# Kernel tuning notes

Measured on AMD Instinct MI355X. Metric: run time of the kernel, lower is better.

The kernel has to match this reference:

```python
import jax, jax.numpy as jnp
import numpy as np

NUM_NODES = 100000
NUM_EDGES = 3200000
NUM_GRAPHS = 512
IN_DIM, OUT_DIM = 128, 16
DIMS = [IN_DIM, 32, 48, 64]


def glorot(key, shape):
    lim = float(np.sqrt(6.0 / (shape[0] + shape[1])))
    return jax.random.uniform(key, shape, jnp.float32, -lim, lim)


def setup_inputs() -> dict:
    key = jax.random.key(0)
    ks = jax.random.split(key, 12)
    x = jax.random.normal(ks[0], (NUM_NODES, IN_DIM), jnp.float32)
    edge_index = jax.random.randint(ks[1], (2, NUM_EDGES), 0, NUM_NODES, jnp.int64)
    batch = jnp.sort(jax.random.randint(ks[2], (NUM_NODES,), 0, NUM_GRAPHS, jnp.int64))
    params = {}
    for i in range(3):
        params[f"W{i+1}"] = glorot(ks[3 + i], (DIMS[i], DIMS[i + 1]))
        params[f"b{i+1}"] = jnp.zeros((DIMS[i + 1],), jnp.float32)
    params["fc1_w"] = glorot(ks[6], (64, 32))
    params["fc1_b"] = jnp.zeros((32,), jnp.float32)
    params["fc2_w"] = glorot(ks[7], (32, OUT_DIM))
    params["fc2_b"] = jnp.zeros((OUT_DIM,), jnp.float32)
    return {"x": x, "edge_index": edge_index, "batch": batch, **params}


def gcn_conv(x, W, b, src, dst, deg_inv_sqrt):
    # h = x @ W; aggregate with symmetric normalization + self loops (PyG GCNConv)
    h = x @ W  # [N, out]
    norm = deg_inv_sqrt[src] * deg_inv_sqrt[dst]  # [E]
    msg = h[src] * norm[:, None]  # [E, out]  (gather)
    agg = jnp.zeros_like(h).at[dst].add(msg)  # scatter-add to targets
    self_loop = h * (deg_inv_sqrt * deg_inv_sqrt)[:, None]
    return agg + self_loop + b


def reference(x, edge_index, batch, W1, b1, W2, b2, W3, b3, fc1_w, fc1_b, fc2_w, fc2_b):
    src, dst = edge_index[0], edge_index[1]
    n = x.shape[0]
    # degree with self loops: deg[i] = in-degree + 1
    deg = jnp.zeros((n,), jnp.float32).at[dst].add(1.0) + 1.0
    dis = jax.lax.rsqrt(deg)
    h = jax.nn.relu(gcn_conv(x, W1, b1, src, dst, dis))
    h = jax.nn.relu(gcn_conv(h, W2, b2, src, dst, dis))
    h = jax.nn.relu(gcn_conv(h, W3, b3, src, dst, dis))
    # global mean pool per graph
    sums = jax.ops.segment_sum(h, batch, num_segments=NUM_GRAPHS)
    cnts = jax.ops.segment_sum(jnp.ones((n,), jnp.float32), batch, num_segments=NUM_GRAPHS)
    pooled = sums / jnp.maximum(cnts, 1.0)[:, None]  # [G, 64]
    z = jax.nn.relu(pooled @ fc1_w + fc1_b)
    logits = z @ fc2_w + fc2_b
    return jax.nn.softmax(logits, axis=1)
```

## Files before the change

### kernel.cpp

```cpp
#include <hip/hip_runtime.h>
#include <hip/hip_fp16.h>

static constexpr int NN = 100000;
static constexpr int NE = 3200000;
static constexpr int NG = 512;
static constexpr int NCB = 196;
static constexpr int CHK = 8192;
static constexpr int NCH = (NE + CHK - 1) / CHK;
static constexpr int NCNT = NCB * NCH;
static constexpr int SCAN_BLK = 2048;
static constexpr int NSB = (NCNT + SCAN_BLK - 1) / SCAN_BLK;

typedef float f32x2 __attribute__((ext_vector_type(2)));

__device__ __forceinline__ void acc_fp8x4(unsigned v, float* a) {
    f32x2 lo = __builtin_amdgcn_cvt_pk_f32_fp8((int)v, false);
    f32x2 hi = __builtin_amdgcn_cvt_pk_f32_fp8((int)v, true);
    a[0] += lo.x; a[1] += lo.y; a[2] += hi.x; a[3] += hi.y;
}
__device__ __forceinline__ void set_fp8x4(unsigned v, float* a) {
    f32x2 lo = __builtin_amdgcn_cvt_pk_f32_fp8((int)v, false);
    f32x2 hi = __builtin_amdgcn_cvt_pk_f32_fp8((int)v, true);
    a[0] = lo.x; a[1] = lo.y; a[2] = hi.x; a[3] = hi.y;
}
__device__ __forceinline__ unsigned pack_fp8x4(float a, float b, float c, float d) {
    int p = __builtin_amdgcn_cvt_pk_fp8_f32(a, b, 0, false);
    p = __builtin_amdgcn_cvt_pk_fp8_f32(c, d, p, true);
    return (unsigned)p;
}

__global__ __launch_bounds__(256) void k_histC(const int* __restrict__ dst,
                                               int* __restrict__ cntC, int e) {
    __shared__ int h[NCB];
    for (int i = threadIdx.x; i < NCB; i += 256) h[i] = 0;
    __syncthreads();
    const int s = blockIdx.x * CHK, eend = min(s + CHK, e);
    for (int i = s + threadIdx.x; i < eend; i += 256)
        atomicAdd(&h[dst[i] >> 9], 1);
    __syncthreads();
    for (int i = threadIdx.x; i < NCB; i += 256)
        cntC[(size_t)i * NCH + blockIdx.x] = h[i];
}

__global__ __launch_bounds__(256) void k_scanA(const int* __restrict__ in,
                                               int* __restrict__ out,
                                               int* __restrict__ bsum, int n) {
    __shared__ int s[256];
    const int tid = threadIdx.x;
    const int base = blockIdx.x * SCAN_BLK + tid * 8;
    int v[8], t = 0;
#pragma unroll
    for (int c = 0; c < 8; c++) {
        int idx = base + c;
        v[c] = (idx < n) ? in[idx] : 0;
        t += v[c];
    }
    s[tid] = t;
    __syncthreads();
    for (int off = 1; off < 256; off <<= 1) {
        int x = (tid >= off) ? s[tid - off] : 0;
        __syncthreads();
        s[tid] += x;
        __syncthreads();
    }
    if (tid == 255) bsum[blockIdx.x] = s[255];
    int run = s[tid] - t;
#pragma unroll
    for (int c = 0; c < 8; c++) {
        int idx = base + c;
        if (idx < n) out[idx] = run;
        run += v[c];
    }
}

__global__ __launch_bounds__(256) void k_scanB(int* __restrict__ bsum, int nb) {
    __shared__ int s[256];
    const int tid = threadIdx.x;
    int v = (tid < nb) ? bsum[tid] : 0;
    s[tid] = v;
    __syncthreads();
    for (int off = 1; off < 256; off <<= 1) {
        int x = (tid >= off) ? s[tid - off] : 0;
        __syncthreads();
        s[tid] += x;
        __syncthreads();
    }
    if (tid < nb) bsum[tid] = s[tid] - v;
}

__global__ __launch_bounds__(256) void k_scanC(int* __restrict__ out,
                                               const int* __restrict__ bsum, int n) {
    int i = blockIdx.x * 256 + threadIdx.x;
    if (i < n) out[i] += bsum[i / SCAN_BLK];
}

__global__ __launch_bounds__(256) void k_scatC(const int* __restrict__ src,
                                               const int* __restrict__ dst,
                                               const int* __restrict__ scC,
                                               unsigned* __restrict__ tmp, int e) {
    __shared__ int cur[NCB];
    for (int i = threadIdx.x; i < NCB; i += 256)
        cur[i] = scC[(size_t)i * NCH + blockIdx.x];
    __syncthreads();
    const int s = blockIdx.x * CHK, eend = min(s + CHK, e);
    for (int i = s + threadIdx.x; i < eend; i += 256) {
        int d = dst[i];
        int p = atomicAdd(&cur[d >> 9], 1);
        tmp[p] = ((unsigned)(d & 511) << 17) | (unsigned)src[i];
    }
}

__global__ __launch_bounds__(1024) void k_fill512(const unsigned* __restrict__ tmp,
                                                  const int* __restrict__ scC,
                                                  int* __restrict__ csr,
                                                  int* __restrict__ degi,
                                                  int* __restrict__ offs,
                                                  float* __restrict__ dis,
                                                  int n, int etotal) {
    __shared__ int cnt[512];
    __shared__ int s[512];
    __shared__ int cur[512];
    const int b = blockIdx.x, tid = threadIdx.x;
    if (tid < 512) cnt[tid] = 0;
    const int e0 = scC[(size_t)b * NCH];
    const int e1 = (b + 1 < NCB) ? scC[(size_t)(b + 1) * NCH] : etotal;
    __syncthreads();
    for (int e = e0 + tid; e < e1; e += 1024)
        atomicAdd(&cnt[tmp[e] >> 17], 1);
    __syncthreads();
    int v = 0;
    if (tid < 512) { v = cnt[tid]; s[tid] = v; }
    __syncthreads();
    for (int off = 1; off < 512; off <<= 1) {
        int x = 0;
        if (tid < 512 && tid >= off) x = s[tid - off];
        __syncthreads();
        if (tid < 512) s[tid] += x;
        __syncthreads();
    }
    if (tid < 512) {
        int c = e0 + s[tid] - v;
        cur[tid] = c;
        int node = b * 512 + tid;
        if (node < n) {
            degi[node] = v;
            offs[node] = c;
            dis[node] = rsqrtf((float)v + 1.0f);
        }
    }
    __syncthreads();
    for (int e = e0 + tid; e < e1; e += 1024) {
        unsigned pk = tmp[e];
        int p = atomicAdd(&cur[pk >> 17], 1);
        csr[p] = (int)(pk & 0x1FFFFu);
    }
}

__global__ __launch_bounds__(256) void k_gemm1(const float* __restrict__ X,
                                               const float* __restrict__ W,
                                               const float* __restrict__ dis,
                                               unsigned* __restrict__ H, int n) {
    constexpr int IN = 128, ROWS = 32;
    __shared__ float sW[IN * 32];
    __shared__ float sX[ROWS][IN];
    const int tid = threadIdx.x;
    for (int i = tid; i < IN * 32; i += 256) sW[i] = W[i];
    const int row0 = blockIdx.x * ROWS;
    for (int i = tid; i < ROWS * IN; i += 256) {
        int r = row0 + i / IN;
        sX[i / IN][i % IN] = (r < n) ? X[(size_t)r * IN + i % IN] : 0.f;
    }
    __syncthreads();
    const int lr = tid >> 3;
    const int cg = tid & 7;
    const int gr = row0 + lr;
    float acc[4] = {0.f, 0.f, 0.f, 0.f};
#pragma unroll 8
    for (int k = 0; k < IN; k++) {
        float xv = sX[lr][k];
#pragma unroll
        for (int c = 0; c < 4; c++)
            acc[c] = fmaf(xv, sW[k * 32 + 4 * cg + c], acc[c]);
    }
    if (gr < n) {
        float dd = dis[gr];
        H[(size_t)gr * 8 + cg] =
            pack_fp8x4(acc[0] * dd, acc[1] * dd, acc[2] * dd, acc[3] * dd);
    }
}

__global__ __launch_bounds__(256) void k_pull2(
        const unsigned* __restrict__ Hp, const int* __restrict__ offs,
        const int* __restrict__ degi, const int* __restrict__ csr,
        const float* __restrict__ dis, const float* __restrict__ b,
        unsigned* __restrict__ A, int n) {
    const int group = threadIdx.x >> 3, j0 = threadIdx.x & 7;
    const int d = blockIdx.x * 32 + group;
    if (d >= n) return;
    float acc[4];
    set_fp8x4(Hp[(size_t)d * 8 + j0], acc);
    int e = offs[d];
    const int end = e + degi[d];
    for (; e + 3 < end; e += 4) {
        unsigned v0 = Hp[(size_t)csr[e] * 8 + j0];
        unsigned v1 = Hp[(size_t)csr[e + 1] * 8 + j0];
        unsigned v2 = Hp[(size_t)csr[e + 2] * 8 + j0];
        unsigned v3 = Hp[(size_t)csr[e + 3] * 8 + j0];
        acc_fp8x4(v0, acc); acc_fp8x4(v1, acc);
        acc_fp8x4(v2, acc); acc_fp8x4(v3, acc);
    }
    for (; e < end; e++) acc_fp8x4(Hp[(size_t)csr[e] * 8 + j0], acc);
    const float dd = dis[d];
    float r[4];
#pragma unroll
    for (int c = 0; c < 4; c++)
        r[c] = fmaxf(fmaf(acc[c], dd, b[4 * j0 + c]), 0.f) * dd;
    A[(size_t)d * 8 + j0] = pack_fp8x4(r[0], r[1], r[2], r[3]);
}

__global__ __launch_bounds__(256) void k_pullmm32(
        const unsigned* __restrict__ Hp, const int* __restrict__ offs,
        const int* __restrict__ degi, const int* __restrict__ csr,
        const float* __restrict__ dis, const float* __restrict__ W,
        const float* __restrict__ b, unsigned* __restrict__ A, int n) {
    __shared__ float sW[32 * 48];
    __shared__ float rows[32][32];
    __shared__ float aout[32][48];
    for (int i = threadIdx.x; i < 32 * 48; i += 256) sW[i] = W[i];
    const int group = threadIdx.x >> 3, j0 = threadIdx.x & 7;
    const int d = blockIdx.x * 32 + group;
    if (d < n) {
        float acc[4];
        set_fp8x4(Hp[(size_t)d * 8 + j0], acc);
        int e = offs[d];
        const int end = e + degi[d];
        for (; e + 3 < end; e += 4) {
            unsigned v0 = Hp[(size_t)csr[e] * 8 + j0];
            unsigned v1 = Hp[(size_t)csr[e + 1] * 8 + j0];
            unsigned v2 = Hp[(size_t)csr[e + 2] * 8 + j0];
            unsigned v3 = Hp[(size_t)csr[e + 3] * 8 + j0];
            acc_fp8x4(v0, acc); acc_fp8x4(v1, acc);
            acc_fp8x4(v2, acc); acc_fp8x4(v3, acc);
        }
        for (; e < end; e++) acc_fp8x4(Hp[(size_t)csr[e] * 8 + j0], acc);
        const float dd = dis[d];
#pragma unroll
        for (int c = 0; c < 4; c++) rows[group][4 * j0 + c] = acc[c] * dd;
    }
    __syncthreads();
    const int row0 = blockIdx.x * 32;
#pragma unroll
    for (int o = 0; o < 6; o++) {
        int idx = o * 256 + threadIdx.x;
        int nl = idx / 48, col = idx % 48;
        float s = b[col];
#pragma unroll
        for (int k = 0; k < 32; k++)
            s = fmaf(rows[nl][k], sW[k * 48 + col], s);
        aout[nl][col] = fmaxf(s, 0.f) * dis[min(row0 + nl, n - 1)];
    }
    __syncthreads();
    for (int idx = threadIdx.x; idx < 32 * 16; idx += 256) {
        int nl = idx >> 4, cg = idx & 15;
        int gr = row0 + nl;
        if (gr < n) {
            unsigned p = 0;
            if (cg < 12)
                p = pack_fp8x4(aout[nl][4 * cg], aout[nl][4 * cg + 1],
                               aout[nl][4 * cg + 2], aout[nl][4 * cg + 3]);
            A[(size_t)gr * 16 + cg] = p;
        }
    }
}

__global__ __launch_bounds__(256) void k_pullmm48(
        const uint2* __restrict__ Hp, const int* __restrict__ offs,
        const int* __restrict__ degi, const int* __restrict__ csr,
        const float* __restrict__ dis, const float* __restrict__ W,
        const float* __restrict__ b, __half* __restrict__ A, int n) {
    __shared__ float sW[48 * 64];
    __shared__ float rows[32][48];
    for (int i = threadIdx.x; i < 48 * 64; i += 256) sW[i] = W[i];
    const int group = threadIdx.x >> 3, j0 = threadIdx.x & 7;
    const int d = blockIdx.x * 32 + group;
    if (d < n) {
        float acc[8];
        uint2 sv = Hp[(size_t)d * 8 + j0];
        set_fp8x4(sv.x, acc); set_fp8x4(sv.y, acc + 4);
        int e = offs[d];
        const int end = e + degi[d];
        for (; e + 3 < end; e += 4) {
            uint2 v0 = Hp[(size_t)csr[e] * 8 + j0];
            uint2 v1 = Hp[(size_t)csr[e + 1] * 8 + j0];
            uint2 v2 = Hp[(size_t)csr[e + 2] * 8 + j0];
            uint2 v3 = Hp[(size_t)csr[e + 3] * 8 + j0];
            acc_fp8x4(v0.x, acc); acc_fp8x4(v0.y, acc + 4);
            acc_fp8x4(v1.x, acc); acc_fp8x4(v1.y, acc + 4);
            acc_fp8x4(v2.x, acc); acc_fp8x4(v2.y, acc + 4);
            acc_fp8x4(v3.x, acc); acc_fp8x4(v3.y, acc + 4);
        }
        for (; e < end; e++) {
            uint2 v = Hp[(size_t)csr[e] * 8 + j0];
            acc_fp8x4(v.x, acc); acc_fp8x4(v.y, acc + 4);
        }
        const float dd = dis[d];
        if (j0 < 6) {
#pragma unroll
            for (int c = 0; c < 8; c++) rows[group][8 * j0 + c] = acc[c] * dd;
        }
    }
    __syncthreads();
    const int row0 = blockIdx.x * 32;
#pragma unroll
    for (int o = 0; o < 8; o++) {
        int idx = o * 256 + threadIdx.x;
        int nl = idx >> 6, col = idx & 63;
        int gr = row0 + nl;
        if (gr < n) {
            float s = b[col];
#pragma unroll
            for (int k = 0; k < 48; k++)
                s = fmaf(rows[nl][k], sW[k * 64 + col], s);
            A[(size_t)gr * 64 + col] = __float2half(s);
        }
    }
}

__global__ __launch_bounds__(256) void k_bounds(const int* __restrict__ batch,
                                                int* __restrict__ bounds,
                                                int n, int ngr) {
    int g = blockIdx.x * 256 + threadIdx.x;
    if (g > ngr) return;
    if (g == ngr) { bounds[g] = n; return; }
    int lo = 0, hi = n;
    while (lo < hi) {
        int mid = (lo + hi) >> 1;
        if (batch[mid] < g) lo = mid + 1; else hi = mid;
    }
    bounds[g] = lo;
}

__global__ __launch_bounds__(256) void k_pool(const __half* __restrict__ A3,
                                              const int* __restrict__ bounds,
                                              float* __restrict__ pooled) {
    const int g = blockIdx.x;
    const int j = threadIdx.x & 63, rl = threadIdx.x >> 6;
    const int s = bounds[g], e = bounds[g + 1];
    float sum = 0.f;
    for (int node = s + rl; node < e; node += 4)
        sum += fmaxf(__half2float(A3[(size_t)node * 64 + j]), 0.f);
    __shared__ float red[4][64];
    red[rl][j] = sum;
    __syncthreads();
    if (rl == 0)
        pooled[g * 64 + j] = (red[0][j] + red[1][j] + red[2][j] + red[3][j]) /
                             fmaxf((float)(e - s), 1.f);
}

__global__ __launch_bounds__(64) void k_head(
        const float* __restrict__ pooled,
        const float* __restrict__ f1w, const float* __restrict__ f1b,
        const float* __restrict__ f2w, const float* __restrict__ f2b,
        float* __restrict__ out) {
    int g = blockIdx.x;
    int t = threadIdx.x;
    __shared__ float p[64], z[32], lg[16];
    p[t] = pooled[g * 64 + t];
    __syncthreads();
    if (t < 32) {
        float acc = f1b[t];
        for (int j = 0; j < 64; j++) acc = fmaf(p[j], f1w[j * 32 + t], acc);
        z[t] = fmaxf(acc, 0.f);
    }
    __syncthreads();
    if (t < 16) {
        float acc = f2b[t];
        for (int k = 0; k < 32; k++) acc = fmaf(z[k], f2w[k * 16 + t], acc);
        lg[t] = acc;
    }
    __syncthreads();
    if (t < 16) {
        float m = lg[0];
        for (int i = 1; i < 16; i++) m = fmaxf(m, lg[i]);
        float s = 0.f;
        for (int i = 0; i < 16; i++) s += expf(lg[i] - m);
        out[g * 16 + t] = expf(lg[t] - m) / s;
    }
}

extern "C" void kernel_launch(void* const* d_in, const int* in_sizes, int n_in,
                              void* d_out, int out_size, void* d_ws, size_t ws_size,
                              hipStream_t stream) {
    (void)in_sizes; (void)n_in; (void)out_size; (void)ws_size;
    const float* x     = (const float*)d_in[0];
    const int*   ei    = (const int*)d_in[1];
    const int*   batch = (const int*)d_in[2];
    const float* W1 = (const float*)d_in[3];
    const float* b1 = (const float*)d_in[4];
    const float* W2 = (const float*)d_in[5];  const float* b2 = (const float*)d_in[6];
    const float* W3 = (const float*)d_in[7];  const float* b3 = (const float*)d_in[8];
    const float* f1w = (const float*)d_in[9]; const float* f1b = (const float*)d_in[10];
    const float* f2w = (const float*)d_in[11];const float* f2b = (const float*)d_in[12];
    float* out = (float*)d_out;

    const int* src = ei;
    const int* dst = ei + NE;

    float* ws = (float*)d_ws;
    size_t o = 0;
    float* dis    = ws + o; o += NN;
    int*   degi   = (int*)(ws + o); o += NN;
    int*   offs   = (int*)(ws + o); o += NN;
    int*   cntC   = (int*)(ws + o); o += 76640;
    int*   scC    = (int*)(ws + o); o += 76640;
    int*   bsum   = (int*)(ws + o); o += 48;
    int*   bounds = (int*)(ws + o); o += 528;
    float* pooled = ws + o; o += (size_t)NG * 64;
    int*   csr    = (int*)(ws + o); o += NE;
    unsigned* TA  = (unsigned*)(ws + o); o += NE;
    unsigned* H1  = (unsigned*)(ws + o); o += NN * 8;
    unsigned* H2  = (unsigned*)(ws + o); o += NN * 8;
    unsigned* H3  = (unsigned*)(ws + o); o += NN * 16;

    unsigned* tmp = TA;
    __half*   A3  = (__half*)TA;

    k_histC<<<NCH, 256, 0, stream>>>(dst, cntC, NE);
    k_scanA<<<NSB, 256, 0, stream>>>(cntC, scC, bsum, NCNT);
    k_scanB<<<1, 256, 0, stream>>>(bsum, NSB);
    k_scanC<<<(NCNT + 255) / 256, 256, 0, stream>>>(scC, bsum, NCNT);
    k_scatC<<<NCH, 256, 0, stream>>>(src, dst, scC, tmp, NE);
    k_fill512<<<NCB, 1024, 0, stream>>>(tmp, scC, csr, degi, offs, dis, NN, NE);

    const int PGRID = (NN + 31) / 32;

    k_gemm1<<<(NN + 31) / 32, 256, 0, stream>>>(x, W1, dis, H1, NN);
    k_pull2<<<PGRID, 256, 0, stream>>>(H1, offs, degi, csr, dis, b1, H2, NN);

    k_pullmm32<<<PGRID, 256, 0, stream>>>(H2, offs, degi, csr, dis, W2, b2, H3, NN);

    k_pullmm48<<<PGRID, 256, 0, stream>>>(
        (const uint2*)H3, offs, degi, csr, dis, W3, b3, A3, NN);

    k_bounds<<<(NG + 1 + 255) / 256, 256, 0, stream>>>(batch, bounds, NN, NG);
    k_pool<<<NG, 256, 0, stream>>>(A3, bounds, pooled);
    k_head<<<NG, 64, 0, stream>>>(pooled, f1w, f1b, f2w, f2b, out);
}
```

Measured before the change: 393.9 us.

## Widen gather loads to 16-byte vectors with fewer lanes per node in pull kernels

The three aggregation kernels now use 2 or 4 lanes per destination node, and each lane loads 16 bytes (uint4) of fp8 features per neighbour instead of 4 or 8 bytes. This gives fewer, wider gather transactions and more nodes per block. CSR index reads use nontemporal loads so they do not pollute the cache. The pullmm32 epilogue is restructured so each thread computes 4 output columns directly, which drops the aout staging buffer and one barrier. In exchange there is more register pressure (16 accumulators per lane) and fewer lanes sharing the edge-loop latency, and the per-lane serial loop over each node's neighbours gets longer.

```diff
diff --git a/kernel.cpp b/kernel.cpp
--- a/kernel.cpp
+++ b/kernel.cpp
@@ -22,6 +22,14 @@
     f32x2 lo = __builtin_amdgcn_cvt_pk_f32_fp8((int)v, false);
     f32x2 hi = __builtin_amdgcn_cvt_pk_f32_fp8((int)v, true);
     a[0] = lo.x; a[1] = lo.y; a[2] = hi.x; a[3] = hi.y;
+}
+__device__ __forceinline__ void acc_u4(uint4 v, float* a) {
+    acc_fp8x4(v.x, a); acc_fp8x4(v.y, a + 4);
+    acc_fp8x4(v.z, a + 8); acc_fp8x4(v.w, a + 12);
+}
+__device__ __forceinline__ void set_u4(uint4 v, float* a) {
+    set_fp8x4(v.x, a); set_fp8x4(v.y, a + 4);
+    set_fp8x4(v.z, a + 8); set_fp8x4(v.w, a + 12);
 }
 __device__ __forceinline__ unsigned pack_fp8x4(float a, float b, float c, float d) {
     int p = __builtin_amdgcn_cvt_pk_fp8_f32(a, b, 0, false);
@@ -190,129 +198,138 @@
 }
 
 __global__ __launch_bounds__(256) void k_pull2(
-        const unsigned* __restrict__ Hp, const int* __restrict__ offs,
+        const uint4* __restrict__ Hp, const int* __restrict__ offs,
         const int* __restrict__ degi, const int* __restrict__ csr,
         const float* __restrict__ dis, const float* __restrict__ b,
-        unsigned* __restrict__ A, int n) {
-    const int group = threadIdx.x >> 3, j0 = threadIdx.x & 7;
-    const int d = blockIdx.x * 32 + group;
+        uint4* __restrict__ A, int n) {
+    const int group = threadIdx.x >> 1, j0 = threadIdx.x & 1;
+    const int d = blockIdx.x * 128 + group;
     if (d >= n) return;
-    float acc[4];
-    set_fp8x4(Hp[(size_t)d * 8 + j0], acc);
+    float acc[16];
+    set_u4(Hp[(size_t)d * 2 + j0], acc);
     int e = offs[d];
     const int end = e + degi[d];
     for (; e + 3 < end; e += 4) {
-        unsigned v0 = Hp[(size_t)csr[e] * 8 + j0];
-        unsigned v1 = Hp[(size_t)csr[e + 1] * 8 + j0];
-        unsigned v2 = Hp[(size_t)csr[e + 2] * 8 + j0];
-        unsigned v3 = Hp[(size_t)csr[e + 3] * 8 + j0];
-        acc_fp8x4(v0, acc); acc_fp8x4(v1, acc);
-        acc_fp8x4(v2, acc); acc_fp8x4(v3, acc);
-    }
-    for (; e < end; e++) acc_fp8x4(Hp[(size_t)csr[e] * 8 + j0], acc);
+        int s0 = __builtin_nontemporal_load(csr + e);
+        int s1 = __builtin_nontemporal_load(csr + e + 1);
+        int s2 = __builtin_nontemporal_load(csr + e + 2);
+        int s3 = __builtin_nontemporal_load(csr + e + 3);
+        uint4 v0 = Hp[(size_t)s0 * 2 + j0];
+        uint4 v1 = Hp[(size_t)s1 * 2 + j0];
+        uint4 v2 = Hp[(size_t)s2 * 2 + j0];
+        uint4 v3 = Hp[(size_t)s3 * 2 + j0];
+        acc_u4(v0, acc); acc_u4(v1, acc); acc_u4(v2, acc); acc_u4(v3, acc);
+    }
+    for (; e < end; e++)
+        acc_u4(Hp[(size_t)__builtin_nontemporal_load(csr + e) * 2 + j0], acc);
     const float dd = dis[d];
-    float r[4];
-#pragma unroll
-    for (int c = 0; c < 4; c++)
-        r[c] = fmaxf(fmaf(acc[c], dd, b[4 * j0 + c]), 0.f) * dd;
-    A[(size_t)d * 8 + j0] = pack_fp8x4(r[0], r[1], r[2], r[3]);
+    float r[16];
+#pragma unroll
+    for (int c = 0; c < 16; c++)
+        r[c] = fmaxf(fmaf(acc[c], dd, b[16 * j0 + c]), 0.f) * dd;
+    uint4 o4;
+    o4.x = pack_fp8x4(r[0], r[1], r[2], r[3]);
+    o4.y = pack_fp8x4(r[4], r[5], r[6], r[7]);
+    o4.z = pack_fp8x4(r[8], r[9], r[10], r[11]);
+    o4.w = pack_fp8x4(r[12], r[13], r[14], r[15]);
+    A[(size_t)d * 2 + j0] = o4;
 }
 
 __global__ __launch_bounds__(256) void k_pullmm32(
-        const unsigned* __restrict__ Hp, const int* __restrict__ offs,
+        const uint4* __restrict__ Hp, const int* __restrict__ offs,
         const int* __restrict__ degi, const int* __restrict__ csr,
         const float* __restrict__ dis, const float* __restrict__ W,
         const float* __restrict__ b, unsigned* __restrict__ A, int n) {
     __shared__ float sW[32 * 48];
-    __shared__ float rows[32][32];
-    __shared__ float aout[32][48];
+    __shared__ float rows[128][34];
     for (int i = threadIdx.x; i < 32 * 48; i += 256) sW[i] = W[i];
-    const int group = threadIdx.x >> 3, j0 = threadIdx.x & 7;
-    const int d = blockIdx.x * 32 + group;
+    const int group = threadIdx.x >> 1, j0 = threadIdx.x & 1;
+    const int d = blockIdx.x * 128 + group;
     if (d < n) {
-        float acc[4];
-        set_fp8x4(Hp[(size_t)d * 8 + j0], acc);
+        float acc[16];
+        set_u4(Hp[(size_t)d * 2 + j0], acc);
         int e = offs[d];
         const int end = e + degi[d];
         for (; e + 3 < end; e += 4) {
-            unsigned v0 = Hp[(size_t)csr[e] * 8 + j0];
-            unsigned v1 = Hp[(size_t)csr[e + 1] * 8 + j0];
-            unsigned v2 = Hp[(size_t)csr[e + 2] * 8 + j0];
-            unsigned v3 = Hp[(size_t)csr[e + 3] * 8 + j0];
-            acc_fp8x4(v0, acc); acc_fp8x4(v1, acc);
-            acc_fp8x4(v2, acc); acc_fp8x4(v3, acc);
-        }
-        for (; e < end; e++) acc_fp8x4(Hp[(size_t)csr[e] * 8 + j0], acc);
+            int s0 = __builtin_nontemporal_load(csr + e);
+            int s1 = __builtin_nontemporal_load(csr + e + 1);
+            int s2 = __builtin_nontemporal_load(csr + e + 2);
+            int s3 = __builtin_nontemporal_load(csr + e + 3);
+            uint4 v0 = Hp[(size_t)s0 * 2 + j0];
+            uint4 v1 = Hp[(size_t)s1 * 2 + j0];
+            uint4 v2 = Hp[(size_t)s2 * 2 + j0];
+            uint4 v3 = Hp[(size_t)s3 * 2 + j0];
+            acc_u4(v0, acc); acc_u4(v1, acc); acc_u4(v2, acc); acc_u4(v3, acc);
+        }
+        for (; e < end; e++)
+            acc_u4(Hp[(size_t)__builtin_nontemporal_load(csr + e) * 2 + j0], acc);
         const float dd = dis[d];
 #pragma unroll
-        for (int c = 0; c < 4; c++) rows[group][4 * j0 + c] = acc[c] * dd;
-    }
-    __syncthreads();
-    const int row0 = blockIdx.x * 32;
-#pragma unroll
-    for (int o = 0; o < 6; o++) {
-        int idx = o * 256 + threadIdx.x;
-        int nl = idx / 48, col = idx % 48;
-        float s = b[col];
-#pragma unroll
-        for (int k = 0; k < 32; k++)
-            s = fmaf(rows[nl][k], sW[k * 48 + col], s);
-        aout[nl][col] = fmaxf(s, 0.f) * dis[min(row0 + nl, n - 1)];
-    }
-    __syncthreads();
-    for (int idx = threadIdx.x; idx < 32 * 16; idx += 256) {
-        int nl = idx >> 4, cg = idx & 15;
+        for (int c = 0; c < 16; c++) rows[group][16 * j0 + c] = acc[c] * dd;
+    }
+    __syncthreads();
+    const int row0 = blockIdx.x * 128;
+    for (int t = threadIdx.x; t < 128 * 16; t += 256) {
+        int nl = t >> 4, cg = t & 15;
         int gr = row0 + nl;
         if (gr < n) {
             unsigned p = 0;
-            if (cg < 12)
-                p = pack_fp8x4(aout[nl][4 * cg], aout[nl][4 * cg + 1],
-                               aout[nl][4 * cg + 2], aout[nl][4 * cg + 3]);
+            if (cg < 12) {
+                float dd2 = dis[gr];
+                float r[4];
+#pragma unroll
+                for (int c = 0; c < 4; c++) {
+                    float s = b[4 * cg + c];
+#pragma unroll
+                    for (int k = 0; k < 32; k++)
+                        s = fmaf(rows[nl][k], sW[k * 48 + 4 * cg + c], s);
+                    r[c] = fmaxf(s, 0.f) * dd2;
+                }
+                p = pack_fp8x4(r[0], r[1], r[2], r[3]);
+            }
             A[(size_t)gr * 16 + cg] = p;
         }
     }
 }
 
 __global__ __launch_bounds__(256) void k_pullmm48(
-        const uint2* __restrict__ Hp, const int* __restrict__ offs,
+        const uint4* __restrict__ Hp, const int* __restrict__ offs,
         const int* __restrict__ degi, const int* __restrict__ csr,
         const float* __restrict__ dis, const float* __restrict__ W,
         const float* __restrict__ b, __half* __restrict__ A, int n) {
     __shared__ float sW[48 * 64];
-    __shared__ float rows[32][48];
+    __shared__ float rows[64][50];
     for (int i = threadIdx.x; i < 48 * 64; i += 256) sW[i] = W[i];
-    const int group = threadIdx.x >> 3, j0 = threadIdx.x & 7;
-    const int d = blockIdx.x * 32 + group;
+    const int group = threadIdx.x >> 2, j0 = threadIdx.x & 3;
+    const int d = blockIdx.x * 64 + group;
     if (d < n) {
-        float acc[8];
-        uint2 sv = Hp[(size_t)d * 8 + j0];
-        set_fp8x4(sv.x, acc); set_fp8x4(sv.y, acc + 4);
+        float acc[16];
+        set_u4(Hp[(size_t)d * 4 + j0], acc);
         int e = offs[d];
         const int end = e + degi[d];
         for (; e + 3 < end; e += 4) {
-            uint2 v0 = Hp[(size_t)csr[e] * 8 + j0];
-            uint2 v1 = Hp[(size_t)csr[e + 1] * 8 + j0];
-            uint2 v2 = Hp[(size_t)csr[e + 2] * 8 + j0];
-            uint2 v3 = Hp[(size_t)csr[e + 3] * 8 + j0];
-            acc_fp8x4(v0.x, acc); acc_fp8x4(v0.y, acc + 4);
-            acc_fp8x4(v1.x, acc); acc_fp8x4(v1.y, acc + 4);
-            acc_fp8x4(v2.x, acc); acc_fp8x4(v2.y, acc + 4);
-            acc_fp8x4(v3.x, acc); acc_fp8x4(v3.y, acc + 4);
-        }
-        for (; e < end; e++) {
-            uint2 v = Hp[(size_t)csr[e] * 8 + j0];
-            acc_fp8x4(v.x, acc); acc_fp8x4(v.y, acc + 4);
-        }
+            int s0 = __builtin_nontemporal_load(csr + e);
+            int s1 = __builtin_nontemporal_load(csr + e + 1);
+            int s2 = __builtin_nontemporal_load(csr + e + 2);
+            int s3 = __builtin_nontemporal_load(csr + e + 3);
+            uint4 v0 = Hp[(size_t)s0 * 4 + j0];
+            uint4 v1 = Hp[(size_t)s1 * 4 + j0];
+            uint4 v2 = Hp[(size_t)s2 * 4 + j0];
+            uint4 v3 = Hp[(size_t)s3 * 4 + j0];
+            acc_u4(v0, acc); acc_u4(v1, acc); acc_u4(v2, acc); acc_u4(v3, acc);
+        }
+        for (; e < end; e++)
+            acc_u4(Hp[(size_t)__builtin_nontemporal_load(csr + e) * 4 + j0], acc);
         const float dd = dis[d];
-        if (j0 < 6) {
-#pragma unroll
-            for (int c = 0; c < 8; c++) rows[group][8 * j0 + c] = acc[c] * dd;
-        }
-    }
-    __syncthreads();
-    const int row0 = blockIdx.x * 32;
-#pragma unroll
-    for (int o = 0; o < 8; o++) {
+        if (j0 < 3) {
+#pragma unroll
+            for (int c = 0; c < 16; c++) rows[group][16 * j0 + c] = acc[c] * dd;
+        }
+    }
+    __syncthreads();
+    const int row0 = blockIdx.x * 64;
+#pragma unroll
+    for (int o = 0; o < 16; o++) {
         int idx = o * 256 + threadIdx.x;
         int nl = idx >> 6, col = idx & 63;
         int gr = row0 + nl;
@@ -432,15 +449,15 @@
     k_scatC<<<NCH, 256, 0, stream>>>(src, dst, scC, tmp, NE);
     k_fill512<<<NCB, 1024, 0, stream>>>(tmp, scC, csr, degi, offs, dis, NN, NE);
 
-    const int PGRID = (NN + 31) / 32;
-
     k_gemm1<<<(NN + 31) / 32, 256, 0, stream>>>(x, W1, dis, H1, NN);
-    k_pull2<<<PGRID, 256, 0, stream>>>(H1, offs, degi, csr, dis, b1, H2, NN);
-
-    k_pullmm32<<<PGRID, 256, 0, stream>>>(H2, offs, degi, csr, dis, W2, b2, H3, NN);
-
-    k_pullmm48<<<PGRID, 256, 0, stream>>>(
-        (const uint2*)H3, offs, degi, csr, dis, W3, b3, A3, NN);
+    k_pull2<<<(NN + 127) / 128, 256, 0, stream>>>(
+        (const uint4*)H1, offs, degi, csr, dis, b1, (uint4*)H2, NN);
+
+    k_pullmm32<<<(NN + 127) / 128, 256, 0, stream>>>(
+        (const uint4*)H2, offs, degi, csr, dis, W2, b2, H3, NN);
+
+    k_pullmm48<<<(NN + 63) / 64, 256, 0, stream>>>(
+        (const uint4*)H3, offs, degi, csr, dis, W3, b3, A3, NN);
 
     k_bounds<<<(NG + 1 + 255) / 256, 256, 0, stream>>>(batch, bounds, NN, NG);
     k_pool<<<NG, 256, 0, stream>>>(A3, bounds, pooled);
```

New measurement: 443.9 us. 1.13x slower.
